# Performance work log

Hardware: AMD Instinct MI355X
Metric: run time of the kernel (lower is better)

Reference implementation:

```python
import jax, jax.numpy as jnp
import numpy as np

HEAD_DIM = 512 // (8 * 2)  # in_dim // (num_heads * 2) = 32
SQRT2 = np.sqrt(2.0).astype(np.float32)


def dwt1d_haar(x):
    # Haar DWT along last dim: L=(even+odd)/sqrt2, H=(even-odd)/sqrt2
    xe, xo = x[..., 0::2], x[..., 1::2]
    return (xe + xo) / SQRT2, (xe - xo) / SQRT2


def idwt1d_haar(L, H):
    # Inverse: even=(L+H)/sqrt2, odd=(L-H)/sqrt2, interleaved
    even = (L + H) / SQRT2
    odd = (L - H) / SQRT2
    x = jnp.stack([even, odd], axis=-1)  # [..., D/2, 2]
    return x.reshape(*x.shape[:-2], -1)  # [..., D]


def setup_inputs() -> dict:
    key = jax.random.key(0)
    k1, k2, k3, k4 = jax.random.split(key, 4)
    B, S, D = 8, 2048, 512
    queries = jax.random.normal(k1, (B, S, D), dtype=jnp.float32)
    keys = jax.random.normal(k2, (B, S, D), dtype=jnp.float32)
    values = jax.random.normal(k3, (B, S, D), dtype=jnp.float32)
    W_o = jax.random.normal(k4, (D, D), dtype=jnp.float32) * (1.0 / np.sqrt(D))
    b_o = jnp.zeros((D,), dtype=jnp.float32)
    return {"queries": queries, "keys": keys, "values": values, "W_o": W_o, "b_o": b_o}


def reference(queries, keys, values, W_o, b_o):
    scale = 1.0 / jnp.sqrt(jnp.asarray(HEAD_DIM, dtype=queries.dtype))
    q_L, q_H = dwt1d_haar(queries)
    k_L, k_H = dwt1d_haar(keys)
    v_L, v_H = dwt1d_haar(values)
    # [B,S,S] score matrices for each wavelet branch
    attn_L = jax.nn.softmax(jnp.einsum("bqd,bkd->bqk", q_L, k_L) * scale, axis=-1)
    attn_H = jax.nn.softmax(jnp.einsum("bqd,bkd->bqk", q_H, k_H) * scale, axis=-1)
    L_out = jnp.einsum("bqk,bkd->bqd", attn_L, v_L)
    H_out = jnp.einsum("bqk,bkd->bqd", attn_H, v_H)
    output = idwt1d_haar(L_out, H_out)  # [B,S,D]
    return output @ W_o.T + b_o
```

## Files before the change

kernel.cpp:

```cpp
#include <hip/hip_runtime.h>

#define INV_SQRT2 0.70710678118654752f
#define QSCALE    0.17677669529663689f
#define LOG2E     1.44269504088896340f
#define SM_HALF   16.0f

typedef __attribute__((ext_vector_type(8))) short bf16x8;
typedef __attribute__((ext_vector_type(4))) float f32x4;
typedef __attribute__((ext_vector_type(16))) float f32x16;

__device__ __forceinline__ unsigned cvt_pk_bf16(float a, float b) {
  unsigned r;
  asm("v_cvt_pk_bf16_f32 %0, %1, %2" : "=v"(r) : "v"(a), "v"(b));
  return r;
}

__device__ __forceinline__ float exp2_raw(float x) {
  float r;
  asm("v_exp_f32 %0, %1" : "=v"(r) : "v"(x));
  return r;
}

__device__ __forceinline__ void async16(const short* g, short* l) {
  typedef __attribute__((address_space(3))) unsigned lds_u32;
  typedef const __attribute__((address_space(1))) unsigned glb_u32;
  __builtin_amdgcn_global_load_lds((glb_u32*)g, (lds_u32*)l, 16, 0, 0);
}

__global__ void dwt_all(const float* __restrict__ q, const float* __restrict__ k,
                        const float* __restrict__ v, const float* __restrict__ W,
                        short* __restrict__ qs, short* __restrict__ ks,
                        short* __restrict__ vt, short* __restrict__ w2) {
  __shared__ short tLb[64][68];
  __shared__ short tHb[64][68];
  int bi = blockIdx.x;
  int t = threadIdx.x;
  if (bi < 2048) {
    int idx = bi * 256 + t;
    int j = idx & 31;
    int s = (idx >> 5) & 2047;
    int b = idx >> 16;
    const float4* qp = (const float4*)(q + ((size_t)(b * 2048 + s)) * 512 + j * 16);
    const float4* kp = (const float4*)(k + ((size_t)(b * 2048 + s)) * 512 + j * 16);
    float4 a0 = qp[0], a1 = qp[1], a2 = qp[2], a3 = qp[3];
    float4 c0 = kp[0], c1 = kp[1], c2 = kp[2], c3 = kp[3];
    union { bf16x8 v; unsigned u[4]; } qL, qH, kL, kH;
    const float cs = INV_SQRT2 * QSCALE * LOG2E;
    qL.u[0] = cvt_pk_bf16((a0.x + a0.y) * cs, (a0.z + a0.w) * cs);
    qL.u[1] = cvt_pk_bf16((a1.x + a1.y) * cs, (a1.z + a1.w) * cs);
    qL.u[2] = cvt_pk_bf16((a2.x + a2.y) * cs, (a2.z + a2.w) * cs);
    qL.u[3] = cvt_pk_bf16((a3.x + a3.y) * cs, (a3.z + a3.w) * cs);
    qH.u[0] = cvt_pk_bf16((a0.x - a0.y) * cs, (a0.z - a0.w) * cs);
    qH.u[1] = cvt_pk_bf16((a1.x - a1.y) * cs, (a1.z - a1.w) * cs);
    qH.u[2] = cvt_pk_bf16((a2.x - a2.y) * cs, (a2.z - a2.w) * cs);
    qH.u[3] = cvt_pk_bf16((a3.x - a3.y) * cs, (a3.z - a3.w) * cs);
    kL.u[0] = cvt_pk_bf16((c0.x + c0.y) * INV_SQRT2, (c0.z + c0.w) * INV_SQRT2);
    kL.u[1] = cvt_pk_bf16((c1.x + c1.y) * INV_SQRT2, (c1.z + c1.w) * INV_SQRT2);
    kL.u[2] = cvt_pk_bf16((c2.x + c2.y) * INV_SQRT2, (c2.z + c2.w) * INV_SQRT2);
    kL.u[3] = cvt_pk_bf16((c3.x + c3.y) * INV_SQRT2, (c3.z + c3.w) * INV_SQRT2);
    kH.u[0] = cvt_pk_bf16((c0.x - c0.y) * INV_SQRT2, (c0.z - c0.w) * INV_SQRT2);
    kH.u[1] = cvt_pk_bf16((c1.x - c1.y) * INV_SQRT2, (c1.z - c1.w) * INV_SQRT2);
    kH.u[2] = cvt_pk_bf16((c2.x - c2.y) * INV_SQRT2, (c2.z - c2.w) * INV_SQRT2);
    kH.u[3] = cvt_pk_bf16((c3.x - c3.y) * INV_SQRT2, (c3.z - c3.w) * INV_SQRT2);
    size_t oL = ((size_t)(b * 2) * 2048 + s) * 256 + j * 8;
    size_t oH = oL + (size_t)2048 * 256;
    *(bf16x8*)(qs + oL) = qL.v;  *(bf16x8*)(qs + oH) = qH.v;
    *(bf16x8*)(ks + oL) = kL.v;  *(bf16x8*)(ks + oH) = kH.v;
  } else if (bi < 3072) {
    int bi2 = bi - 2048;
    int it = bi2 & 3, st = (bi2 >> 2) & 31, b = bi2 >> 7;
    const float* vsrc = v + ((size_t)(b * 2048 + st * 64)) * 512 + it * 128;
#pragma unroll
    for (int rep = 0; rep < 8; rep++) {
      int u = rep * 256 + t;
      int r = u >> 5, c4 = u & 31;
      float4 vv = *(const float4*)(vsrc + (size_t)r * 512 + c4 * 4);
      *(unsigned*)&tLb[r][c4 * 2] = cvt_pk_bf16((vv.x + vv.y) * INV_SQRT2, (vv.z + vv.w) * INV_SQRT2);
      *(unsigned*)&tHb[r][c4 * 2] = cvt_pk_bf16((vv.x - vv.y) * INV_SQRT2, (vv.z - vv.w) * INV_SQRT2);
    }
    __syncthreads();
    short* vtb = vt + ((size_t)(b * 2) * 256 + it * 64) * 2048 + st * 64;
#pragma unroll
    for (int rep = 0; rep < 2; rep++) {
      int u = rep * 256 + t;
      int ip = u & 31, g = (u >> 5) & 7, lh = u >> 8;
      const short (*tile)[68] = lh ? tHb : tLb;
      union { bf16x8 v; unsigned short e[8]; } o0, o1;
#pragma unroll
      for (int j = 0; j < 8; j++) {
        unsigned wv = *(const unsigned*)&tile[g * 8 + j][ip * 2];
        o0.e[j] = (unsigned short)wv;
        o1.e[j] = (unsigned short)(wv >> 16);
      }
      short* dst = vtb + (size_t)lh * 256 * 2048 + (size_t)(ip * 2) * 2048 + g * 8;
      *(bf16x8*)dst = o0.v;
      *(bf16x8*)(dst + 2048) = o1.v;
    }
  } else {
    int idx = (bi - 3072) * 256 + t;
    int j = idx >> 6, i4 = (idx & 63) * 4;
    const float4* src = (const float4*)(W + (size_t)j * 512 + 2 * i4);
    float4 f0 = src[0], f1 = src[1];
    uint2 dl, dh;
    dl.x = cvt_pk_bf16((f0.x + f0.y) * INV_SQRT2, (f0.z + f0.w) * INV_SQRT2);
    dl.y = cvt_pk_bf16((f1.x + f1.y) * INV_SQRT2, (f1.z + f1.w) * INV_SQRT2);
    dh.x = cvt_pk_bf16((f0.x - f0.y) * INV_SQRT2, (f0.z - f0.w) * INV_SQRT2);
    dh.y = cvt_pk_bf16((f1.x - f1.y) * INV_SQRT2, (f1.z - f1.w) * INV_SQRT2);
    *(uint2*)(w2 + (size_t)j * 512 + i4) = dl;
    *(uint2*)(w2 + (size_t)j * 512 + 256 + i4) = dh;
  }
}

__launch_bounds__(256, 2)
__global__ void flash_attn(const short* __restrict__ qs, const short* __restrict__ ks,
                           const short* __restrict__ vt, short* __restrict__ os) {
  __shared__ short lds[36864];
  short* klds = lds;
  short* vlds = lds + 16384;
  short* plds = lds + 32768;

  int tid = threadIdx.x;
  int w = tid >> 6, L = tid & 63;
  int lq = L & 31, hi = L >> 5;
  int qt = w & 1, ct = w >> 1;
  int bb = blockIdx.x, qb = blockIdx.y;

  bf16x8 qf[16];
  const short* qptr = qs + (((size_t)bb * 2048) + qb * 64 + qt * 32 + lq) * 256 + hi * 8;
#pragma unroll
  for (int ksI = 0; ksI < 16; ksI++)
    qf[ksI] = *(const bf16x8*)(qptr + ksI * 16);

  f32x16 oacc[4];
#pragma unroll
  for (int mt = 0; mt < 4; mt++)
#pragma unroll
    for (int i = 0; i < 16; i++) oacc[mt][i] = 0.f;
  float l_i = 0.f;

  const short* kbase = ks + ((size_t)bb * 2048) * 256;
  const short* vbase = vt + ((size_t)bb * 256) * 2048;

  int krow = ct * 32 + lq, ksw = krow & 7;
  int qrow = qt * 32 + lq, qsw = qrow & 7;
  int sw8 = lq & 7;

  const short* kaddr[16];
#pragma unroll
  for (int i = 0; i < 16; i++)
    kaddr[i] = klds + krow * 256 + (((i << 1) | hi) ^ ksw) * 8;
  short* pwr[4];
#pragma unroll
  for (int g = 0; g < 4; g++)
    pwr[g] = plds + qrow * 64 + ((4 * ct + g) ^ qsw) * 8 + hi * 4;
  const short* prdA[4];
  const short* prdB[4];
#pragma unroll
  for (int i = 0; i < 4; i++) {
    int ch = (((i << 1) | hi) ^ sw8) * 8;
    prdA[i] = plds + lq * 64 + ch;
    prdB[i] = plds + (32 + lq) * 64 + ch;
  }
  int vch[4];
#pragma unroll
  for (int i = 0; i < 4; i++)
    vch[i] = (((i << 1) | hi) ^ sw8) * 8;
  const short* vrowp[2];
#pragma unroll
  for (int dt = 0; dt < 2; dt++)
    vrowp[dt] = vlds + (w * 64 + dt * 32 + lq) * 64;

  const short* kp[8];
  const short* vp[8];
#pragma unroll
  for (int rep = 0; rep < 8; rep++) {
    int o = w * 8 + rep;
    int r = 2 * o + (L >> 5);
    int c = (L & 31) ^ (r & 7);
    kp[rep] = kbase + r * 256 + c * 8;
    int n = 8 * o + (L >> 3);
    int cv = (L & 7) ^ (n & 7);
    vp[rep] = vbase + n * 2048 + cv * 8;
  }

#pragma unroll
  for (int rep = 0; rep < 8; rep++) {
    async16(kp[rep], klds + (w * 8 + rep) * 512);
    kp[rep] += 16384;
  }
  __syncthreads();

  for (int kt = 0; kt < 32; kt++) {
#pragma unroll
    for (int rep = 0; rep < 8; rep++) {
      async16(vp[rep], vlds + (w * 8 + rep) * 512);
      vp[rep] += 64;
    }

    f32x16 s0, s1;
#pragma unroll
    for (int i = 0; i < 16; i++) { s0[i] = -SM_HALF; s1[i] = -SM_HALF; }
    __builtin_amdgcn_s_setprio(1);
#pragma unroll
    for (int ksI = 0; ksI < 16; ksI += 2) {
      bf16x8 kb0 = *(const bf16x8*)kaddr[ksI];
      bf16x8 kb1 = *(const bf16x8*)kaddr[ksI + 1];
      s0 = __builtin_amdgcn_mfma_f32_32x32x16_bf16(kb0, qf[ksI], s0, 0, 0, 0);
      s1 = __builtin_amdgcn_mfma_f32_32x32x16_bf16(kb1, qf[ksI + 1], s1, 0, 0, 0);
    }
    __builtin_amdgcn_s_setprio(0);

    float rs = 0.f;
#pragma unroll
    for (int g = 0; g < 4; g++) {
      float p0 = exp2_raw(s0[4 * g]     + s1[4 * g]);
      float p1 = exp2_raw(s0[4 * g + 1] + s1[4 * g + 1]);
      float p2 = exp2_raw(s0[4 * g + 2] + s1[4 * g + 2]);
      float p3 = exp2_raw(s0[4 * g + 3] + s1[4 * g + 3]);
      rs += (p0 + p1) + (p2 + p3);
      uint2 d; d.x = cvt_pk_bf16(p0, p1); d.y = cvt_pk_bf16(p2, p3);
      *(uint2*)pwr[g] = d;
    }
    l_i += rs;
    __syncthreads();

    if (kt < 31) {
#pragma unroll
      for (int rep = 0; rep < 8; rep++) {
        async16(kp[rep], klds + (w * 8 + rep) * 512);
        kp[rep] += 16384;
      }
    }

    bf16x8 pa[4], pb[4];
#pragma unroll
    for (int i = 0; i < 4; i++) {
      pa[i] = *(const bf16x8*)prdA[i];
      pb[i] = *(const bf16x8*)prdB[i];
    }
    __builtin_amdgcn_s_setprio(1);
#pragma unroll
    for (int dt = 0; dt < 2; dt++) {
#pragma unroll
      for (int i = 0; i < 4; i++) {
        bf16x8 vb = *(const bf16x8*)(vrowp[dt] + vch[i]);
        oacc[dt * 2]     = __builtin_amdgcn_mfma_f32_32x32x16_bf16(vb, pa[i], oacc[dt * 2], 0, 0, 0);
        oacc[dt * 2 + 1] = __builtin_amdgcn_mfma_f32_32x32x16_bf16(vb, pb[i], oacc[dt * 2 + 1], 0, 0, 0);
      }
    }
    __builtin_amdgcn_s_setprio(0);
    __syncthreads();
  }

  float lt = l_i + __shfl_xor(l_i, 32, 64);
  float* lbuf = (float*)plds;
  if (hi == 0) lbuf[(ct * 2 + qt) * 32 + lq] = lt;
  __syncthreads();
  float inv0 = 1.f / (lbuf[lq] + lbuf[64 + lq]);
  float inv1 = 1.f / (lbuf[32 + lq] + lbuf[96 + lq]);

#pragma unroll
  for (int ot = 0; ot < 4; ot++) {
    int qt2 = ot & 1, dt = ot >> 1;
    float inv = qt2 ? inv1 : inv0;
    int qg = qt2 * 32 + lq;
#pragma unroll
    for (int g = 0; g < 4; g++) {
      uint2 d;
      d.x = cvt_pk_bf16(oacc[ot][4 * g] * inv, oacc[ot][4 * g + 1] * inv);
      d.y = cvt_pk_bf16(oacc[ot][4 * g + 2] * inv, oacc[ot][4 * g + 3] * inv);
      *(uint2*)(lds + qg * 264 + w * 64 + dt * 32 + 8 * g + 4 * hi) = d;
    }
  }
  __syncthreads();
  short* obase = os + (((size_t)bb * 2048) + qb * 64) * 256;
#pragma unroll
  for (int rep = 0; rep < 8; rep++) {
    int cid = rep * 256 + tid;
    int row = cid >> 5, c = cid & 31;
    *(bf16x8*)(obase + row * 256 + c * 8) = *(const bf16x8*)(lds + row * 264 + c * 8);
  }
}

__launch_bounds__(256, 3)
__global__ void out_gemm(const short* __restrict__ os, const short* __restrict__ w2,
                         const float* __restrict__ bo, float* __restrict__ out) {
  __shared__ short alds[2][4096];
  __shared__ short blds[2][8192];
  int tid = threadIdx.x;
  int w = tid >> 6, L = tid & 63, lo = L & 15, hi = L >> 4;
  int wr = w >> 1, wc = w & 1;
  int br = blockIdx.x, bc = blockIdx.y;

  int arow[2], achk[2];
#pragma unroll
  for (int rep = 0; rep < 2; rep++) {
    int o = w * 2 + rep;
    int r = o * 8 + (L >> 3);
    arow[rep] = r;
    achk[rep] = ((L & 7) ^ (r & 7)) * 8;
  }
  int brow[4], bchk[4];
#pragma unroll
  for (int rep = 0; rep < 4; rep++) {
    int o = w * 4 + rep;
    int r = o * 8 + (L >> 3);
    brow[rep] = r;
    bchk[rep] = ((L & 7) ^ (r & 7)) * 8;
  }
  int b = br >> 5;
  int s0 = (br & 31) * 64;
  const short* abase = os + ((size_t)(b * 2) * 2048 + s0) * 256;
  const short* bbase = w2 + (size_t)(bc * 128) * 512;

  f32x4 acc[2][4];
#pragma unroll
  for (int mt = 0; mt < 2; mt++)
#pragma unroll
    for (int nt = 0; nt < 4; nt++)
      acc[mt][nt] = (f32x4){0.f, 0.f, 0.f, 0.f};

  int fch[2];
#pragma unroll
  for (int kc = 0; kc < 2; kc++)
    fch[kc] = ((kc * 4 + hi) ^ (lo & 7)) * 8;

#pragma unroll
  for (int rep = 0; rep < 2; rep++)
    async16(abase + arow[rep] * 256 + achk[rep], &alds[0][(w * 2 + rep) * 512] + L * 8);
#pragma unroll
  for (int rep = 0; rep < 4; rep++)
    async16(bbase + brow[rep] * 512 + bchk[rep], &blds[0][(w * 4 + rep) * 512] + L * 8);
  __syncthreads();

  int p = 0;
  for (int kt = 0; kt < 8; kt++) {
    if (kt < 7) {
      int k1 = kt + 1;
      int half = k1 >> 2, i0 = (k1 & 3) * 64;
      const short* ab = abase + (size_t)half * 2048 * 256 + i0;
#pragma unroll
      for (int rep = 0; rep < 2; rep++)
        async16(ab + arow[rep] * 256 + achk[rep], &alds[p ^ 1][(w * 2 + rep) * 512] + L * 8);
#pragma unroll
      for (int rep = 0; rep < 4; rep++)
        async16(bbase + brow[rep] * 512 + k1 * 64 + bchk[rep], &blds[p ^ 1][(w * 4 + rep) * 512] + L * 8);
    }
    bf16x8 af[2], bfr[4];
#pragma unroll
    for (int kc = 0; kc < 2; kc++) {
#pragma unroll
      for (int mt = 0; mt < 2; mt++)
        af[mt] = *(const bf16x8*)(&alds[p][(wr * 32 + mt * 16 + lo) * 64 + fch[kc]]);
#pragma unroll
      for (int nt = 0; nt < 4; nt++)
        bfr[nt] = *(const bf16x8*)(&blds[p][(wc * 64 + nt * 16 + lo) * 64 + fch[kc]]);
#pragma unroll
      for (int mt = 0; mt < 2; mt++)
#pragma unroll
        for (int nt = 0; nt < 4; nt++)
          acc[mt][nt] = __builtin_amdgcn_mfma_f32_16x16x32_bf16(af[mt], bfr[nt], acc[mt][nt], 0, 0, 0);
    }
    __syncthreads();
    p ^= 1;
  }

#pragma unroll
  for (int nt = 0; nt < 4; nt++) {
    int cc = bc * 128 + wc * 64 + nt * 16 + lo;
    float bias = bo[cc];
#pragma unroll
    for (int mt = 0; mt < 2; mt++) {
      int rrbase = br * 64 + wr * 32 + mt * 16 + hi * 4;
#pragma unroll
      for (int r = 0; r < 4; r++)
        out[(size_t)(rrbase + r) * 512 + cc] = acc[mt][nt][r] + bias;
    }
  }
}

extern "C" void kernel_launch(void* const* d_in, const int* in_sizes, int n_in,
                              void* d_out, int out_size, void* d_ws, size_t ws_size,
                              hipStream_t stream) {
  const float* q  = (const float*)d_in[0];
  const float* k  = (const float*)d_in[1];
  const float* v  = (const float*)d_in[2];
  const float* W  = (const float*)d_in[3];
  const float* bo = (const float*)d_in[4];
  short* ws  = (short*)d_ws;
  short* qs  = ws;
  short* ksb = ws + (size_t)8  * 1024 * 1024;
  short* vtp = ws + (size_t)16 * 1024 * 1024;
  short* osb = ws + (size_t)24 * 1024 * 1024;
  short* w2  = ws + (size_t)32 * 1024 * 1024;

  dwt_all<<<3200, 256, 0, stream>>>(q, k, v, W, qs, ksb, vtp, w2);
  flash_attn<<<dim3(16, 32), 256, 0, stream>>>(qs, ksb, vtp, osb);
  out_gemm<<<dim3(256, 4), 256, 0, stream>>>(osb, w2, bo, (float*)d_out);
}
```

Before: 241.8 us.

## Prefetch K tiles directly into registers instead of staging through LDS

K fragments now come straight from global memory into registers with inline global_load_dwordx4, prefetched one iteration ahead. This removes the K buffer from shared memory and the LDS reads for the QK^T MFMAs. Synchronisation is rewritten as explicit s_waitcnt vmcnt counts plus raw s_barrier in place of __syncthreads. The gain in exchange is lower LDS usage and traffic. The cost is more VGPR pressure from holding 16 extra bf16x8 registers, each wave re-reading K rows from global or L2 without sharing across waves, and fragile hand-counted vmcnt values that must match the async V loads.

```diff
diff --git a/kernel.cpp b/kernel.cpp
--- a/kernel.cpp
+++ b/kernel.cpp
@@ -26,6 +26,30 @@
   typedef const __attribute__((address_space(1))) unsigned glb_u32;
   __builtin_amdgcn_global_load_lds((glb_u32*)g, (lds_u32*)l, 16, 0, 0);
 }
+
+#define KPRE(PTR)                                                         \
+  asm volatile(                                                           \
+    "global_load_dwordx4 %0, %16, off\n\t"                                \
+    "global_load_dwordx4 %1, %16, off offset:32\n\t"                      \
+    "global_load_dwordx4 %2, %16, off offset:64\n\t"                      \
+    "global_load_dwordx4 %3, %16, off offset:96\n\t"                      \
+    "global_load_dwordx4 %4, %16, off offset:128\n\t"                     \
+    "global_load_dwordx4 %5, %16, off offset:160\n\t"                     \
+    "global_load_dwordx4 %6, %16, off offset:192\n\t"                     \
+    "global_load_dwordx4 %7, %16, off offset:224\n\t"                     \
+    "global_load_dwordx4 %8, %16, off offset:256\n\t"                     \
+    "global_load_dwordx4 %9, %16, off offset:288\n\t"                     \
+    "global_load_dwordx4 %10, %16, off offset:320\n\t"                    \
+    "global_load_dwordx4 %11, %16, off offset:352\n\t"                    \
+    "global_load_dwordx4 %12, %16, off offset:384\n\t"                    \
+    "global_load_dwordx4 %13, %16, off offset:416\n\t"                    \
+    "global_load_dwordx4 %14, %16, off offset:448\n\t"                    \
+    "global_load_dwordx4 %15, %16, off offset:480\n\t"                    \
+    : "=&v"(kf[0]), "=&v"(kf[1]), "=&v"(kf[2]), "=&v"(kf[3]),             \
+      "=&v"(kf[4]), "=&v"(kf[5]), "=&v"(kf[6]), "=&v"(kf[7]),             \
+      "=&v"(kf[8]), "=&v"(kf[9]), "=&v"(kf[10]), "=&v"(kf[11]),           \
+      "=&v"(kf[12]), "=&v"(kf[13]), "=&v"(kf[14]), "=&v"(kf[15])          \
+    : "v"(PTR) : "memory")
 
 __global__ void dwt_all(const float* __restrict__ q, const float* __restrict__ k,
                         const float* __restrict__ v, const float* __restrict__ W,
@@ -114,10 +138,9 @@
 __launch_bounds__(256, 2)
 __global__ void flash_attn(const short* __restrict__ qs, const short* __restrict__ ks,
                            const short* __restrict__ vt, short* __restrict__ os) {
-  __shared__ short lds[36864];
-  short* klds = lds;
-  short* vlds = lds + 16384;
-  short* plds = lds + 32768;
+  __shared__ short lds[20480];
+  short* vlds = lds;
+  short* plds = lds + 16384;
 
   int tid = threadIdx.x;
   int w = tid >> 6, L = tid & 63;
@@ -141,61 +164,39 @@
   const short* kbase = ks + ((size_t)bb * 2048) * 256;
   const short* vbase = vt + ((size_t)bb * 256) * 2048;
 
-  int krow = ct * 32 + lq, ksw = krow & 7;
   int qrow = qt * 32 + lq, qsw = qrow & 7;
   int sw8 = lq & 7;
 
-  const short* kaddr[16];
-#pragma unroll
-  for (int i = 0; i < 16; i++)
-    kaddr[i] = klds + krow * 256 + (((i << 1) | hi) ^ ksw) * 8;
   short* pwr[4];
 #pragma unroll
   for (int g = 0; g < 4; g++)
     pwr[g] = plds + qrow * 64 + ((4 * ct + g) ^ qsw) * 8 + hi * 4;
-  const short* prdA[4];
-  const short* prdB[4];
-#pragma unroll
-  for (int i = 0; i < 4; i++) {
-    int ch = (((i << 1) | hi) ^ sw8) * 8;
-    prdA[i] = plds + lq * 64 + ch;
-    prdB[i] = plds + (32 + lq) * 64 + ch;
-  }
+  const short* prd[4];
+#pragma unroll
+  for (int i = 0; i < 4; i++)
+    prd[i] = plds + lq * 64 + (((i << 1) | hi) ^ sw8) * 8;
   int vch[4];
 #pragma unroll
   for (int i = 0; i < 4; i++)
     vch[i] = (((i << 1) | hi) ^ sw8) * 8;
-  const short* vrowp[2];
-#pragma unroll
-  for (int dt = 0; dt < 2; dt++)
-    vrowp[dt] = vlds + (w * 64 + dt * 32 + lq) * 64;
-
-  const short* kp[8];
-  const short* vp[8];
-#pragma unroll
-  for (int rep = 0; rep < 8; rep++) {
-    int o = w * 8 + rep;
-    int r = 2 * o + (L >> 5);
-    int c = (L & 31) ^ (r & 7);
-    kp[rep] = kbase + r * 256 + c * 8;
-    int n = 8 * o + (L >> 3);
-    int cv = (L & 7) ^ (n & 7);
-    vp[rep] = vbase + n * 2048 + cv * 8;
-  }
-
-#pragma unroll
-  for (int rep = 0; rep < 8; rep++) {
-    async16(kp[rep], klds + (w * 8 + rep) * 512);
-    kp[rep] += 16384;
-  }
-  __syncthreads();
+  const short* vrow0 = vlds + (w * 64 + lq) * 64;
+
+  const short* vbL = vbase + (size_t)(64 * w + (L >> 3)) * 2048
+                           + ((L & 7) ^ ((L >> 3) & 7)) * 8;
+
+  const short* kl0 = kbase + (size_t)(ct * 32 + lq) * 256 + hi * 8;
+
+  bf16x8 kf[16];
+  KPRE(kl0);
 
   for (int kt = 0; kt < 32; kt++) {
 #pragma unroll
-    for (int rep = 0; rep < 8; rep++) {
-      async16(vp[rep], vlds + (w * 8 + rep) * 512);
-      vp[rep] += 64;
-    }
+    for (int rep = 0; rep < 8; rep++)
+      async16(vbL + rep * 16384, vlds + (w * 8 + rep) * 512);
+    vbL += 64;
+
+    asm volatile("s_waitcnt vmcnt(8)" ::: "memory");
+    __builtin_amdgcn_sched_barrier(0);
 
     f32x16 s0, s1;
 #pragma unroll
@@ -203,12 +204,16 @@
     __builtin_amdgcn_s_setprio(1);
 #pragma unroll
     for (int ksI = 0; ksI < 16; ksI += 2) {
-      bf16x8 kb0 = *(const bf16x8*)kaddr[ksI];
-      bf16x8 kb1 = *(const bf16x8*)kaddr[ksI + 1];
-      s0 = __builtin_amdgcn_mfma_f32_32x32x16_bf16(kb0, qf[ksI], s0, 0, 0, 0);
-      s1 = __builtin_amdgcn_mfma_f32_32x32x16_bf16(kb1, qf[ksI + 1], s1, 0, 0, 0);
+      s0 = __builtin_amdgcn_mfma_f32_32x32x16_bf16(kf[ksI], qf[ksI], s0, 0, 0, 0);
+      s1 = __builtin_amdgcn_mfma_f32_32x32x16_bf16(kf[ksI + 1], qf[ksI + 1], s1, 0, 0, 0);
     }
     __builtin_amdgcn_s_setprio(0);
+    __builtin_amdgcn_sched_barrier(0);
+
+    {
+      const short* kpre = kl0 + (size_t)((kt + 1) & 31) * 16384;
+      KPRE(kpre);
+    }
 
     float rs = 0.f;
 #pragma unroll
@@ -222,38 +227,36 @@
       *(uint2*)pwr[g] = d;
     }
     l_i += rs;
-    __syncthreads();
-
-    if (kt < 31) {
-#pragma unroll
-      for (int rep = 0; rep < 8; rep++) {
-        async16(kp[rep], klds + (w * 8 + rep) * 512);
-        kp[rep] += 16384;
-      }
-    }
+
+    asm volatile("s_waitcnt vmcnt(16) lgkmcnt(0)" ::: "memory");
+    __builtin_amdgcn_s_barrier();
+    __builtin_amdgcn_sched_barrier(0);
 
     bf16x8 pa[4], pb[4];
 #pragma unroll
     for (int i = 0; i < 4; i++) {
-      pa[i] = *(const bf16x8*)prdA[i];
-      pb[i] = *(const bf16x8*)prdB[i];
+      pa[i] = *(const bf16x8*)prd[i];
+      pb[i] = *(const bf16x8*)(prd[i] + 2048);
     }
     __builtin_amdgcn_s_setprio(1);
 #pragma unroll
     for (int dt = 0; dt < 2; dt++) {
 #pragma unroll
       for (int i = 0; i < 4; i++) {
-        bf16x8 vb = *(const bf16x8*)(vrowp[dt] + vch[i]);
+        bf16x8 vb = *(const bf16x8*)(vrow0 + dt * 2048 + vch[i]);
         oacc[dt * 2]     = __builtin_amdgcn_mfma_f32_32x32x16_bf16(vb, pa[i], oacc[dt * 2], 0, 0, 0);
         oacc[dt * 2 + 1] = __builtin_amdgcn_mfma_f32_32x32x16_bf16(vb, pb[i], oacc[dt * 2 + 1], 0, 0, 0);
       }
     }
     __builtin_amdgcn_s_setprio(0);
-    __syncthreads();
+
+    asm volatile("s_waitcnt lgkmcnt(0)" ::: "memory");
+    __builtin_amdgcn_s_barrier();
+    __builtin_amdgcn_sched_barrier(0);
   }
 
   float lt = l_i + __shfl_xor(l_i, 32, 64);
-  float* lbuf = (float*)plds;
+  float* lbuf = (float*)(lds + 16896);
   if (hi == 0) lbuf[(ct * 2 + qt) * 32 + lq] = lt;
   __syncthreads();
   float inv0 = 1.f / (lbuf[lq] + lbuf[64 + lq]);
```

Result: slower. 332.8 us (+37.6%).
